# Kernel tuning notes

Hardware: AMD Instinct MI355X
Metric: run time of the kernel (lower is better)

The kernel has to match this reference:

```python
import jax, jax.numpy as jnp
import numpy as np

N_NODES = 50000
N_EDGES = 800000
IN_FEAT = 128
H_FEAT = 64
NUM_HEADS = 4
NEG_SLOPE = 0.2  # DGL GATConv default LeakyReLU slope


def _gat_conv(feat, src, dst, W, attn_l, attn_r, bias, num_heads, out_feats):
    # feat: [N, Din]; W: [Din, H*F]; attn_l/attn_r: [H, F]; bias: [H*F]
    N = feat.shape[0]
    h = (feat @ W).reshape(N, num_heads, out_feats)          # [N, H, F]
    el = jnp.sum(h * attn_l, axis=-1)                        # [N, H]
    er = jnp.sum(h * attn_r, axis=-1)                        # [N, H]
    e = jax.nn.leaky_relu(el[src] + er[dst], NEG_SLOPE)      # [E, H]
    # segment softmax over incoming edges of each destination node
    m = jax.ops.segment_max(e, dst, num_segments=N)          # [N, H]
    ex = jnp.exp(e - m[dst])                                 # [E, H]
    s = jax.ops.segment_sum(ex, dst, num_segments=N)         # [N, H]
    alpha = ex / s[dst]                                      # [E, H]
    # attn_drop omitted (eval-mode deterministic reference)
    msg = h[src] * alpha[:, :, None]                         # [E, H, F]
    out = jax.ops.segment_sum(msg, dst, num_segments=N)      # [N, H, F]
    return out + bias.reshape(1, num_heads, out_feats)


def setup_inputs() -> dict:
    key = jax.random.key(0)
    ks = jax.random.split(key, 16)
    feat = jax.random.normal(ks[0], (N_NODES, IN_FEAT), dtype=jnp.float32)
    src = jax.random.randint(ks[1], (N_EDGES,), 0, N_NODES)
    dst = jax.random.randint(ks[2], (N_EDGES,), 0, N_NODES)
    sc = 0.1
    H, F = NUM_HEADS, H_FEAT
    params = {
        'W1': jax.random.normal(ks[3], (IN_FEAT, H * F), dtype=jnp.float32) * sc,
        'al1': jax.random.normal(ks[4], (H, F), dtype=jnp.float32) * sc,
        'ar1': jax.random.normal(ks[5], (H, F), dtype=jnp.float32) * sc,
        'b1': jnp.zeros((H * F,), dtype=jnp.float32),
        'W2': jax.random.normal(ks[6], (H * F, H * F), dtype=jnp.float32) * sc,
        'al2': jax.random.normal(ks[7], (H, F), dtype=jnp.float32) * sc,
        'ar2': jax.random.normal(ks[8], (H, F), dtype=jnp.float32) * sc,
        'b2': jnp.zeros((H * F,), dtype=jnp.float32),
        'W3': jax.random.normal(ks[9], (H * F, F), dtype=jnp.float32) * sc,
        'al3': jax.random.normal(ks[10], (1, F), dtype=jnp.float32) * sc,
        'ar3': jax.random.normal(ks[11], (1, F), dtype=jnp.float32) * sc,
        'b3': jnp.zeros((F,), dtype=jnp.float32),
    }
    return {'feat': feat, 'src': src, 'dst': dst, **params}


def reference(feat, src, dst, W1, al1, ar1, b1, W2, al2, ar2, b2, W3, al3, ar3, b3):
    h = _gat_conv(feat, src, dst, W1, al1, ar1, b1, NUM_HEADS, H_FEAT)
    h = jax.nn.relu(h.reshape(h.shape[0], -1))               # flatten(1) + relu
    h = _gat_conv(h, src, dst, W2, al2, ar2, b2, NUM_HEADS, H_FEAT)
    h = jax.nn.relu(h.reshape(h.shape[0], -1))
    h = _gat_conv(h, src, dst, W3, al3, ar3, b3, 1, H_FEAT)
    return h.mean(axis=1)                                    # [N, h_feat]
```

## Files before the change

kernel.cpp:

```cpp
#include <hip/hip_runtime.h>
#include <math.h>

#define N_NODES 50000
#define N_EDGES 800000

typedef short bf8 __attribute__((ext_vector_type(8)));
typedef float f4x __attribute__((ext_vector_type(4)));
typedef float f2v __attribute__((ext_vector_type(2)));
typedef unsigned short us8 __attribute__((ext_vector_type(8)));

__device__ __forceinline__ unsigned short f2bf(float x) {
  unsigned u = __float_as_uint(x);
  unsigned r = (u + 0x7fff + ((u >> 16) & 1)) >> 16;
  return (unsigned short)r;
}
__device__ __forceinline__ float bf2f(unsigned short b) {
  return __uint_as_float(((unsigned)b) << 16);
}
__device__ __forceinline__ f2v bfpair(unsigned d) {
  f2v r;
  r.x = __uint_as_float(d << 16);
  r.y = __uint_as_float(d & 0xffff0000u);
  return r;
}

__global__ __launch_bounds__(256) void feat_cvt_k(
    const float* __restrict__ in, unsigned short* __restrict__ out,
    int total8) {
  int i = blockIdx.x * 256 + threadIdx.x;
  if (i < total8) {
    float4 a = ((const float4*)in)[2 * i];
    float4 b = ((const float4*)in)[2 * i + 1];
    us8 o;
    o[0] = f2bf(a.x); o[1] = f2bf(a.y); o[2] = f2bf(a.z); o[3] = f2bf(a.w);
    o[4] = f2bf(b.x); o[5] = f2bf(b.y); o[6] = f2bf(b.z); o[7] = f2bf(b.w);
    ((us8*)out)[i] = o;
  }
}

__global__ __launch_bounds__(256) void wt_cvt_k(
    const float* __restrict__ W, unsigned short* __restrict__ WT, int K,
    int M) {
  int i = blockIdx.x * 256 + threadIdx.x;
  int k8n = K >> 3;
  if (i < M * k8n) {
    int m = i / k8n, k8 = i - m * k8n;
    us8 o;
#pragma unroll
    for (int r = 0; r < 8; ++r) o[r] = f2bf(W[(size_t)(k8 * 8 + r) * M + m]);
    *(us8*)(WT + (size_t)m * K + k8 * 8) = o;
  }
}

__global__ __launch_bounds__(256) void gemm_mfma_k(
    const unsigned short* __restrict__ Xb, const unsigned short* __restrict__ WT,
    unsigned short* __restrict__ Yb, float* __restrict__ el,
    float* __restrict__ er, const float* __restrict__ al,
    const float* __restrict__ ar, int N, int K, int M) {
  __shared__ unsigned short As[128][40];
  __shared__ unsigned short Bs[64][40];
  const int tile_n = blockIdx.x * 128;
  const int cb = blockIdx.y * 64;
  const int t = threadIdx.x;
  const int wave = t >> 6, lane = t & 63;
  const int quad = lane >> 4, l16 = lane & 15;

  f4x acc[2][4];
#pragma unroll
  for (int i = 0; i < 2; ++i)
#pragma unroll
    for (int j = 0; j < 4; ++j) acc[i][j] = (f4x){0.f, 0.f, 0.f, 0.f};

  const int ar_ = t >> 1;
  const int ac0 = (t & 1) * 16;
  const int bn = t >> 2;
  const int bk0 = (t & 3) * 8;

  for (int k0 = 0; k0 < K; k0 += 32) {
    {
      int gr = tile_n + ar_;
      us8 u0 = (us8)0;
      if (gr < N) u0 = *(const us8*)(Xb + (size_t)gr * K + k0 + ac0);
      *(us8*)&As[ar_][ac0] = u0;
      us8 u1 = (us8)0;
      if (gr < N) u1 = *(const us8*)(Xb + (size_t)gr * K + k0 + ac0 + 8);
      *(us8*)&As[ar_][ac0 + 8] = u1;
    }
    {
      us8 w = *(const us8*)(WT + (size_t)(cb + bn) * K + k0 + bk0);
      *(us8*)&Bs[bn][bk0] = w;
    }
    __syncthreads();
    bf8 afrag[2], bfrag[4];
#pragma unroll
    for (int rt = 0; rt < 2; ++rt)
      afrag[rt] = *(const bf8*)&As[wave * 32 + rt * 16 + l16][quad * 8];
#pragma unroll
    for (int ct = 0; ct < 4; ++ct)
      bfrag[ct] = *(const bf8*)&Bs[ct * 16 + l16][quad * 8];
#pragma unroll
    for (int rt = 0; rt < 2; ++rt)
#pragma unroll
      for (int ct = 0; ct < 4; ++ct)
        acc[rt][ct] = __builtin_amdgcn_mfma_f32_16x16x32_bf16(
            afrag[rt], bfrag[ct], acc[rt][ct], 0, 0, 0);
    __syncthreads();
  }
  const int H = M >> 6;
  const int head = cb >> 6;
  float al4[4], ar4[4];
#pragma unroll
  for (int ct = 0; ct < 4; ++ct) {
    al4[ct] = al[cb + ct * 16 + l16];
    ar4[ct] = ar[cb + ct * 16 + l16];
  }
#pragma unroll
  for (int rt = 0; rt < 2; ++rt) {
#pragma unroll
    for (int r = 0; r < 4; ++r) {
      int row = tile_n + wave * 32 + rt * 16 + quad * 4 + r;
      float pl = 0.f, pr = 0.f;
#pragma unroll
      for (int ct = 0; ct < 4; ++ct) {
        float y = acc[rt][ct][r];
        pl += y * al4[ct];
        pr += y * ar4[ct];
        if (row < N) Yb[(size_t)row * M + cb + ct * 16 + l16] = f2bf(y);
      }
#pragma unroll
      for (int off = 1; off < 16; off <<= 1) {
        pl += __shfl_xor(pl, off);
        pr += __shfl_xor(pr, off);
      }
      if (l16 == 0 && row < N) {
        el[row * H + head] = pl;
        er[row * H + head] = pr;
      }
    }
  }
}

__global__ __launch_bounds__(256) void count_deg_k(
    const int4* __restrict__ dst4, int* __restrict__ deg, int E4) {
  int i = blockIdx.x * blockDim.x + threadIdx.x;
  if (i < E4) {
    int4 d = dst4[i];
    atomicAdd(&deg[d.x], 1);
    atomicAdd(&deg[d.y], 1);
    atomicAdd(&deg[d.z], 1);
    atomicAdd(&deg[d.w], 1);
  }
}

__global__ __launch_bounds__(256) void alloc_rows_k(
    const int* __restrict__ deg, int* __restrict__ rowstart,
    int* __restrict__ cursor, int* __restrict__ gcounter, int N) {
  int i = blockIdx.x * blockDim.x + threadIdx.x;
  int lane = threadIdx.x & 63;
  int d = (i < N) ? deg[i] : 0;
  int x = d;
#pragma unroll
  for (int off = 1; off < 64; off <<= 1) {
    int t = __shfl_up(x, off);
    if (lane >= off) x += t;
  }
  int wsum = __shfl(x, 63);
  int base = 0;
  if (lane == 63) base = atomicAdd(gcounter, wsum);
  base = __shfl(base, 63);
  if (i < N) {
    int mystart = base + x - d;
    rowstart[i] = mystart;
    cursor[i] = mystart;
  }
}

__global__ __launch_bounds__(256) void scatter_k(
    const int4* __restrict__ src4, const int4* __restrict__ dst4,
    int* __restrict__ cursor, int* __restrict__ src_sorted, int E4) {
  int i = blockIdx.x * blockDim.x + threadIdx.x;
  if (i < E4) {
    int4 s = src4[i];
    int4 d = dst4[i];
    int p0 = atomicAdd(&cursor[d.x], 1);
    src_sorted[p0] = s.x;
    int p1 = atomicAdd(&cursor[d.y], 1);
    src_sorted[p1] = s.y;
    int p2 = atomicAdd(&cursor[d.z], 1);
    src_sorted[p2] = s.z;
    int p3 = atomicAdd(&cursor[d.w], 1);
    src_sorted[p3] = s.w;
  }
}

template <int RELU>
__global__ __launch_bounds__(256) void node_agg4_k(
    const unsigned short* __restrict__ hb, const float* __restrict__ el,
    const float* __restrict__ er, const int* __restrict__ rowstart,
    const int* __restrict__ rowend, const int* __restrict__ src_sorted,
    const float* __restrict__ bias, unsigned short* __restrict__ outb,
    int N) {
  int node = blockIdx.x * 4 + (threadIdx.x >> 6);
  int lane = threadIdx.x & 63;
  if (node >= N) return;
  int start = rowstart[node], end = rowend[node];
  int e16 = lane & 15;
  int headA = lane >> 4;
  int eslot = lane >> 5;
  int flane = lane & 31;
  int fo8 = flane << 3;
  int headf = fo8 >> 6;
  float er_a = er[node * 4 + headA];
  f2v acc2[4];
#pragma unroll
  for (int q = 0; q < 4; ++q) acc2[q] = (f2v){0.f, 0.f};
  float ssum = 0.f;
  for (int c0 = start; c0 < end; c0 += 16) {
    int p = c0 + e16;
    bool v = p < end;
    int s = v ? src_sorted[p] : 0;
    float e = el[s * 4 + headA] + er_a;
    e = (e >= 0.f) ? e : 0.2f * e;
    float ex = v ? __expf(e) : 0.f;
    ssum += ex;
    int sjv[8];
    float ajv[8];
#pragma unroll
    for (int jj = 0; jj < 8; ++jj) {
      int idx = (2 * jj + eslot) | (headf << 4);
      sjv[jj] = __shfl(s, idx);
      ajv[jj] = __shfl(ex, idx);
    }
    int nch = end - c0;
    if (nch > 16) nch = 16;
    int nj = (nch + 1) >> 1;
#pragma unroll 8
    for (int jj = 0; jj < nj; ++jj) {
      uint4 d = *(const uint4*)(hb + (size_t)sjv[jj] * 256 + fo8);
      f2v a2 = (f2v){ajv[jj], ajv[jj]};
      acc2[0] += bfpair(d.x) * a2;
      acc2[1] += bfpair(d.y) * a2;
      acc2[2] += bfpair(d.z) * a2;
      acc2[3] += bfpair(d.w) * a2;
    }
  }
#pragma unroll
  for (int off = 1; off < 16; off <<= 1) ssum += __shfl_xor(ssum, off);
  float sden = __shfl(ssum, headf << 4);
  float acc[8];
#pragma unroll
  for (int q = 0; q < 4; ++q) {
    acc[2 * q] = acc2[q].x;
    acc[2 * q + 1] = acc2[q].y;
  }
#pragma unroll
  for (int q = 0; q < 8; ++q) acc[q] += __shfl_xor(acc[q], 32);
  float inv = (end > start) ? 1.f / sden : 0.f;
  if (eslot == 0) {
    us8 o;
#pragma unroll
    for (int q = 0; q < 8; ++q) {
      float vv = acc[q] * inv + bias[fo8 + q];
      if (RELU) vv = fmaxf(vv, 0.f);
      o[q] = f2bf(vv);
    }
    *(us8*)(outb + (size_t)node * 256 + fo8) = o;
  }
}

__global__ __launch_bounds__(256) void node_agg1_k(
    const unsigned short* __restrict__ hb, const float* __restrict__ el,
    const float* __restrict__ er, const int* __restrict__ rowstart,
    const int* __restrict__ rowend, const int* __restrict__ src_sorted,
    const float* __restrict__ bias, float* __restrict__ out, int N) {
  int node = blockIdx.x * 4 + (threadIdx.x >> 6);
  int lane = threadIdx.x & 63;
  if (node >= N) return;
  int start = rowstart[node], end = rowend[node];
  int eslot = lane >> 3;
  int fo8 = (lane & 7) << 3;
  float er_v = er[node];
  f2v acc2[4];
#pragma unroll
  for (int q = 0; q < 4; ++q) acc2[q] = (f2v){0.f, 0.f};
  float ssum = 0.f;
  for (int c0 = start; c0 < end; c0 += 64) {
    int p = c0 + lane;
    bool v = p < end;
    int s = v ? src_sorted[p] : 0;
    float e = el[s] + er_v;
    e = (e >= 0.f) ? e : 0.2f * e;
    float ex = v ? __expf(e) : 0.f;
    ssum += ex;
    int nch = end - c0;
    if (nch > 64) nch = 64;
    int nj = (nch + 7) >> 3;
#pragma unroll 8
    for (int jj = 0; jj < nj; ++jj) {
      int idx = jj * 8 + eslot;
      int sj = __shfl(s, idx);
      float aj = __shfl(ex, idx);
      uint4 d = *(const uint4*)(hb + (size_t)sj * 64 + fo8);
      f2v a2 = (f2v){aj, aj};
      acc2[0] += bfpair(d.x) * a2;
      acc2[1] += bfpair(d.y) * a2;
      acc2[2] += bfpair(d.z) * a2;
      acc2[3] += bfpair(d.w) * a2;
    }
  }
#pragma unroll
  for (int off = 1; off < 64; off <<= 1) ssum += __shfl_xor(ssum, off);
  float acc[8];
#pragma unroll
  for (int q = 0; q < 4; ++q) {
    acc[2 * q] = acc2[q].x;
    acc[2 * q + 1] = acc2[q].y;
  }
#pragma unroll
  for (int off = 8; off < 64; off <<= 1)
#pragma unroll
    for (int q = 0; q < 8; ++q) acc[q] += __shfl_xor(acc[q], off);
  float inv = (end > start) ? 1.f / ssum : 0.f;
  if (eslot == 0) {
    float* o = out + (size_t)node * 64 + fo8;
#pragma unroll
    for (int q = 0; q < 8; ++q) o[q] = acc[q] * inv + bias[fo8 + q];
  }
}

extern "C" void kernel_launch(void* const* d_in, const int* in_sizes, int n_in,
                              void* d_out, int out_size, void* d_ws,
                              size_t ws_size, hipStream_t stream) {
  const float* feat = (const float*)d_in[0];
  const int* src = (const int*)d_in[1];
  const int* dst = (const int*)d_in[2];
  const float* W1 = (const float*)d_in[3];
  const float* al1 = (const float*)d_in[4];
  const float* ar1 = (const float*)d_in[5];
  const float* b1 = (const float*)d_in[6];
  const float* W2 = (const float*)d_in[7];
  const float* al2 = (const float*)d_in[8];
  const float* ar2 = (const float*)d_in[9];
  const float* b2 = (const float*)d_in[10];
  const float* W3 = (const float*)d_in[11];
  const float* al3 = (const float*)d_in[12];
  const float* ar3 = (const float*)d_in[13];
  const float* b3 = (const float*)d_in[14];
  float* out = (float*)d_out;

  unsigned short* hb = (unsigned short*)d_ws;
  unsigned short* fb = hb + (size_t)N_NODES * 256;
  float* el = (float*)(fb + (size_t)N_NODES * 256);
  float* er = el + (size_t)N_NODES * 4;
  int* rowstart = (int*)(er + (size_t)N_NODES * 4);
  int* cursor = rowstart + N_NODES;
  int* deg = cursor + N_NODES;
  int* gcounter = deg + N_NODES;
  int* src_sorted = gcounter + 1;
  unsigned short* wt1 = (unsigned short*)(src_sorted + N_EDGES);
  unsigned short* wt2 = wt1 + 128 * 256;
  unsigned short* wt3 = wt2 + 256 * 256;
  unsigned short* featb = fb;

  const int N = N_NODES, E = N_EDGES;
  const int E4 = E / 4;
  const int GX = (N + 127) / 128;

  hipLaunchKernelGGL(feat_cvt_k, dim3((N * 128 / 8 + 255) / 256), dim3(256), 0,
                     stream, feat, featb, N * 128 / 8);
  hipLaunchKernelGGL(wt_cvt_k, dim3((256 * 16 + 255) / 256), dim3(256), 0,
                     stream, W1, wt1, 128, 256);
  hipLaunchKernelGGL(wt_cvt_k, dim3((256 * 32 + 255) / 256), dim3(256), 0,
                     stream, W2, wt2, 256, 256);
  hipLaunchKernelGGL(wt_cvt_k, dim3((64 * 32 + 255) / 256), dim3(256), 0,
                     stream, W3, wt3, 256, 64);

  hipMemsetAsync(deg, 0, (size_t)(N + 1) * sizeof(int), stream);
  hipLaunchKernelGGL(count_deg_k, dim3((E4 + 255) / 256), dim3(256), 0, stream,
                     (const int4*)dst, deg, E4);
  hipLaunchKernelGGL(alloc_rows_k, dim3((N + 255) / 256), dim3(256), 0, stream,
                     deg, rowstart, cursor, gcounter, N);
  hipLaunchKernelGGL(scatter_k, dim3((E4 + 255) / 256), dim3(256), 0, stream,
                     (const int4*)src, (const int4*)dst, cursor, src_sorted,
                     E4);

  hipLaunchKernelGGL(gemm_mfma_k, dim3(GX, 4), dim3(256), 0, stream, featb,
                     wt1, hb, el, er, al1, ar1, N, 128, 256);
  hipLaunchKernelGGL((node_agg4_k<1>), dim3((N + 3) / 4), dim3(256), 0, stream,
                     hb, el, er, rowstart, cursor, src_sorted, b1, fb, N);

  hipLaunchKernelGGL(gemm_mfma_k, dim3(GX, 4), dim3(256), 0, stream, fb, wt2,
                     hb, el, er, al2, ar2, N, 256, 256);
  hipLaunchKernelGGL((node_agg4_k<1>), dim3((N + 3) / 4), dim3(256), 0, stream,
                     hb, el, er, rowstart, cursor, src_sorted, b2, fb, N);

  hipLaunchKernelGGL(gemm_mfma_k, dim3(GX, 1), dim3(256), 0, stream, fb, wt3,
                     hb, el, er, al3, ar3, N, 256, 64);
  hipLaunchKernelGGL(node_agg1_k, dim3((N + 3) / 4), dim3(256), 0, stream, hb,
                     el, er, rowstart, cursor, src_sorted, b3, out, N);
}
```

Before: 422.1 us.

## Retile GEMM to full output width per block and merge conversion kernels

```diff
diff --git a/kernel.cpp b/kernel.cpp
--- a/kernel.cpp
+++ b/kernel.cpp
@@ -24,117 +24,129 @@
   return r;
 }
 
-__global__ __launch_bounds__(256) void feat_cvt_k(
-    const float* __restrict__ in, unsigned short* __restrict__ out,
-    int total8) {
+__device__ __forceinline__ void wt_cvt_one(const float* __restrict__ W,
+                                           unsigned short* __restrict__ WT,
+                                           int K, int M, int j) {
+  int k8n = K >> 3;
+  int m = j / k8n, k8 = j - m * k8n;
+  us8 o;
+#pragma unroll
+  for (int r = 0; r < 8; ++r) o[r] = f2bf(W[(size_t)(k8 * 8 + r) * M + m]);
+  *(us8*)(WT + (size_t)m * K + k8 * 8) = o;
+}
+
+__global__ __launch_bounds__(256) void cvt_all_k(
+    const float* __restrict__ feat, unsigned short* __restrict__ featb,
+    const float* __restrict__ W1, unsigned short* __restrict__ wt1,
+    const float* __restrict__ W2, unsigned short* __restrict__ wt2,
+    const float* __restrict__ W3, unsigned short* __restrict__ wt3) {
+  const int F8 = N_NODES * 128 / 8;
   int i = blockIdx.x * 256 + threadIdx.x;
-  if (i < total8) {
-    float4 a = ((const float4*)in)[2 * i];
-    float4 b = ((const float4*)in)[2 * i + 1];
+  if (i < F8) {
+    float4 a = ((const float4*)feat)[2 * i];
+    float4 b = ((const float4*)feat)[2 * i + 1];
     us8 o;
     o[0] = f2bf(a.x); o[1] = f2bf(a.y); o[2] = f2bf(a.z); o[3] = f2bf(a.w);
     o[4] = f2bf(b.x); o[5] = f2bf(b.y); o[6] = f2bf(b.z); o[7] = f2bf(b.w);
-    ((us8*)out)[i] = o;
-  }
-}
-
-__global__ __launch_bounds__(256) void wt_cvt_k(
-    const float* __restrict__ W, unsigned short* __restrict__ WT, int K,
-    int M) {
-  int i = blockIdx.x * 256 + threadIdx.x;
-  int k8n = K >> 3;
-  if (i < M * k8n) {
-    int m = i / k8n, k8 = i - m * k8n;
-    us8 o;
-#pragma unroll
-    for (int r = 0; r < 8; ++r) o[r] = f2bf(W[(size_t)(k8 * 8 + r) * M + m]);
-    *(us8*)(WT + (size_t)m * K + k8 * 8) = o;
-  }
-}
-
+    ((us8*)featb)[i] = o;
+    return;
+  }
+  int j = i - F8;
+  if (j < 4096) {
+    wt_cvt_one(W1, wt1, 128, 256, j);
+    return;
+  }
+  j -= 4096;
+  if (j < 8192) {
+    wt_cvt_one(W2, wt2, 256, 256, j);
+    return;
+  }
+  j -= 8192;
+  if (j < 2048) {
+    wt_cvt_one(W3, wt3, 256, 64, j);
+  }
+}
+
+template <int NCT>
 __global__ __launch_bounds__(256) void gemm_mfma_k(
-    const unsigned short* __restrict__ Xb, const unsigned short* __restrict__ WT,
-    unsigned short* __restrict__ Yb, float* __restrict__ el,
-    float* __restrict__ er, const float* __restrict__ al,
-    const float* __restrict__ ar, int N, int K, int M) {
-  __shared__ unsigned short As[128][40];
-  __shared__ unsigned short Bs[64][40];
-  const int tile_n = blockIdx.x * 128;
-  const int cb = blockIdx.y * 64;
+    const unsigned short* __restrict__ Xb,
+    const unsigned short* __restrict__ WT, unsigned short* __restrict__ Yb,
+    float* __restrict__ el, float* __restrict__ er,
+    const float* __restrict__ al, const float* __restrict__ ar, int N,
+    int K) {
+  const int M = NCT * 16;
+  const int H = NCT >> 2;
+  __shared__ unsigned short As[64][40];
+  __shared__ unsigned short Bs[NCT * 16][40];
+  const int tile_n = blockIdx.x * 64;
   const int t = threadIdx.x;
   const int wave = t >> 6, lane = t & 63;
   const int quad = lane >> 4, l16 = lane & 15;
 
-  f4x acc[2][4];
-#pragma unroll
-  for (int i = 0; i < 2; ++i)
-#pragma unroll
-    for (int j = 0; j < 4; ++j) acc[i][j] = (f4x){0.f, 0.f, 0.f, 0.f};
-
-  const int ar_ = t >> 1;
-  const int ac0 = (t & 1) * 16;
-  const int bn = t >> 2;
-  const int bk0 = (t & 3) * 8;
+  f4x acc[NCT];
+#pragma unroll
+  for (int ct = 0; ct < NCT; ++ct) acc[ct] = (f4x){0.f, 0.f, 0.f, 0.f};
+
+  const int arow = t >> 2;
+  const int akoff = (t & 3) * 8;
 
   for (int k0 = 0; k0 < K; k0 += 32) {
     {
-      int gr = tile_n + ar_;
-      us8 u0 = (us8)0;
-      if (gr < N) u0 = *(const us8*)(Xb + (size_t)gr * K + k0 + ac0);
-      *(us8*)&As[ar_][ac0] = u0;
-      us8 u1 = (us8)0;
-      if (gr < N) u1 = *(const us8*)(Xb + (size_t)gr * K + k0 + ac0 + 8);
-      *(us8*)&As[ar_][ac0 + 8] = u1;
-    }
-    {
-      us8 w = *(const us8*)(WT + (size_t)(cb + bn) * K + k0 + bk0);
-      *(us8*)&Bs[bn][bk0] = w;
+      int gr = tile_n + arow;
+      us8 a = (us8)0;
+      if (gr < N) a = *(const us8*)(Xb + (size_t)gr * K + k0 + akoff);
+      *(us8*)&As[arow][akoff] = a;
+    }
+#pragma unroll
+    for (int u = 0; u < NCT / 4; ++u) {
+      int g = t + u * 256;
+      int brow = g >> 2, bk = (g & 3) * 8;
+      *(us8*)&Bs[brow][bk] = *(const us8*)(WT + (size_t)brow * K + k0 + bk);
     }
     __syncthreads();
-    bf8 afrag[2], bfrag[4];
-#pragma unroll
-    for (int rt = 0; rt < 2; ++rt)
-      afrag[rt] = *(const bf8*)&As[wave * 32 + rt * 16 + l16][quad * 8];
-#pragma unroll
-    for (int ct = 0; ct < 4; ++ct)
-      bfrag[ct] = *(const bf8*)&Bs[ct * 16 + l16][quad * 8];
-#pragma unroll
-    for (int rt = 0; rt < 2; ++rt)
-#pragma unroll
-      for (int ct = 0; ct < 4; ++ct)
-        acc[rt][ct] = __builtin_amdgcn_mfma_f32_16x16x32_bf16(
-            afrag[rt], bfrag[ct], acc[rt][ct], 0, 0, 0);
+    bf8 afrag = *(const bf8*)&As[wave * 16 + l16][quad * 8];
+#pragma unroll
+    for (int ct = 0; ct < NCT; ++ct) {
+      bf8 bfrag = *(const bf8*)&Bs[ct * 16 + l16][quad * 8];
+      acc[ct] = __builtin_amdgcn_mfma_f32_16x16x32_bf16(afrag, bfrag, acc[ct],
+                                                        0, 0, 0);
+    }
     __syncthreads();
   }
-  const int H = M >> 6;
-  const int head = cb >> 6;
-  float al4[4], ar4[4];
-#pragma unroll
-  for (int ct = 0; ct < 4; ++ct) {
-    al4[ct] = al[cb + ct * 16 + l16];
-    ar4[ct] = ar[cb + ct * 16 + l16];
-  }
-#pragma unroll
-  for (int rt = 0; rt < 2; ++rt) {
-#pragma unroll
-    for (int r = 0; r < 4; ++r) {
-      int row = tile_n + wave * 32 + rt * 16 + quad * 4 + r;
-      float pl = 0.f, pr = 0.f;
-#pragma unroll
-      for (int ct = 0; ct < 4; ++ct) {
-        float y = acc[rt][ct][r];
-        pl += y * al4[ct];
-        pr += y * ar4[ct];
-        if (row < N) Yb[(size_t)row * M + cb + ct * 16 + l16] = f2bf(y);
+  float al4[NCT], ar4[NCT];
+#pragma unroll
+  for (int ct = 0; ct < NCT; ++ct) {
+    al4[ct] = al[ct * 16 + l16];
+    ar4[ct] = ar[ct * 16 + l16];
+  }
+#pragma unroll
+  for (int r = 0; r < 4; ++r) {
+    int row = tile_n + wave * 16 + quad * 4 + r;
+    float pl[H], pr[H];
+#pragma unroll
+    for (int h = 0; h < H; ++h) {
+      pl[h] = 0.f;
+      pr[h] = 0.f;
+    }
+#pragma unroll
+    for (int ct = 0; ct < NCT; ++ct) {
+      float y = acc[ct][r];
+      pl[ct >> 2] += y * al4[ct];
+      pr[ct >> 2] += y * ar4[ct];
+      if (row < N) Yb[(size_t)row * M + ct * 16 + l16] = f2bf(y);
+    }
+#pragma unroll
+    for (int off = 1; off < 16; off <<= 1)
+#pragma unroll
+      for (int h = 0; h < H; ++h) {
+        pl[h] += __shfl_xor(pl[h], off);
+        pr[h] += __shfl_xor(pr[h], off);
       }
-#pragma unroll
-      for (int off = 1; off < 16; off <<= 1) {
-        pl += __shfl_xor(pl, off);
-        pr += __shfl_xor(pr, off);
-      }
-      if (l16 == 0 && row < N) {
-        el[row * H + head] = pl;
-        er[row * H + head] = pr;
+    if (l16 == 0 && row < N) {
+#pragma unroll
+      for (int h = 0; h < H; ++h) {
+        el[row * H + h] = pl[h];
+        er[row * H + h] = pr[h];
       }
     }
   }
@@ -358,22 +370,17 @@
   int* gcounter = deg + N_NODES;
   int* src_sorted = gcounter + 1;
   unsigned short* wt1 = (unsigned short*)(src_sorted + N_EDGES);
-  unsigned short* wt2 = wt1 + 128 * 256;
+  unsigned short* wt2 = wt1 + 256 * 128;
   unsigned short* wt3 = wt2 + 256 * 256;
   unsigned short* featb = fb;
 
   const int N = N_NODES, E = N_EDGES;
   const int E4 = E / 4;
-  const int GX = (N + 127) / 128;
-
-  hipLaunchKernelGGL(feat_cvt_k, dim3((N * 128 / 8 + 255) / 256), dim3(256), 0,
-                     stream, feat, featb, N * 128 / 8);
-  hipLaunchKernelGGL(wt_cvt_k, dim3((256 * 16 + 255) / 256), dim3(256), 0,
-                     stream, W1, wt1, 128, 256);
-  hipLaunchKernelGGL(wt_cvt_k, dim3((256 * 32 + 255) / 256), dim3(256), 0,
-                     stream, W2, wt2, 256, 256);
-  hipLaunchKernelGGL(wt_cvt_k, dim3((64 * 32 + 255) / 256), dim3(256), 0,
-                     stream, W3, wt3, 256, 64);
+  const int GX = (N + 63) / 64;
+
+  const int CVT_TOTAL = N * 128 / 8 + 4096 + 8192 + 2048;
+  hipLaunchKernelGGL(cvt_all_k, dim3((CVT_TOTAL + 255) / 256), dim3(256), 0,
+                     stream, feat, featb, W1, wt1, W2, wt2, W3, wt3);
 
   hipMemsetAsync(deg, 0, (size_t)(N + 1) * sizeof(int), stream);
   hipLaunchKernelGGL(count_deg_k, dim3((E4 + 255) / 256), dim3(256), 0, stream,
@@ -384,18 +391,18 @@
                      (const int4*)src, (const int4*)dst, cursor, src_sorted,
                      E4);
 
-  hipLaunchKernelGGL(gemm_mfma_k, dim3(GX, 4), dim3(256), 0, stream, featb,
-                     wt1, hb, el, er, al1, ar1, N, 128, 256);
+  hipLaunchKernelGGL((gemm_mfma_k<16>), dim3(GX), dim3(256), 0, stream, featb,
+                     wt1, hb, el, er, al1, ar1, N, 128);
   hipLaunchKernelGGL((node_agg4_k<1>), dim3((N + 3) / 4), dim3(256), 0, stream,
                      hb, el, er, rowstart, cursor, src_sorted, b1, fb, N);
 
-  hipLaunchKernelGGL(gemm_mfma_k, dim3(GX, 4), dim3(256), 0, stream, fb, wt2,
-                     hb, el, er, al2, ar2, N, 256, 256);
+  hipLaunchKernelGGL((gemm_mfma_k<16>), dim3(GX), dim3(256), 0, stream, fb,
+                     wt2, hb, el, er, al2, ar2, N, 256);
   hipLaunchKernelGGL((node_agg4_k<1>), dim3((N + 3) / 4), dim3(256), 0, stream,
                      hb, el, er, rowstart, cursor, src_sorted, b2, fb, N);
 
-  hipLaunchKernelGGL(gemm_mfma_k, dim3(GX, 1), dim3(256), 0, stream, fb, wt3,
-                     hb, el, er, al3, ar3, N, 256, 64);
+  hipLaunchKernelGGL((gemm_mfma_k<4>), dim3(GX), dim3(256), 0, stream, fb, wt3,
+                     hb, el, er, al3, ar3, N, 256);
   hipLaunchKernelGGL(node_agg1_k, dim3((N + 3) / 4), dim3(256), 0, stream, hb,
                      el, er, rowstart, cursor, src_sorted, b3, out, N);
 }
```

Measured after the change: 426.1 us. Within noise of the previous version (+1.0%).
